# Kernel optimization log

Measured on AMD Instinct MI355X. Metric: run time of the kernel, lower is better.

## Reference

```python
import jax, jax.numpy as jnp
import numpy as np

B, S, D = 4, 2048, 1024
H, DK = 16, 64
NUM_BUCKETS = 32
MAX_DISTANCE = 128
EPS = 1e-6


def _relative_position_bucket(q_len, kv_len):
    # causal (bidirectional=False) T5 bucketization
    ctx = jnp.arange(q_len, dtype=jnp.int32)[:, None]
    mem = jnp.arange(kv_len, dtype=jnp.int32)[None, :]
    rp = mem - ctx                       # [q, kv]
    rp = -jnp.minimum(rp, 0)             # nonnegative distances to the past
    max_exact = NUM_BUCKETS // 2
    is_small = rp < max_exact
    rp_safe = jnp.maximum(rp, 1).astype(jnp.float32)
    large = max_exact + (
        jnp.log(rp_safe / max_exact) / np.log(MAX_DISTANCE / max_exact) * (NUM_BUCKETS - max_exact)
    ).astype(jnp.int32)
    large = jnp.minimum(large, NUM_BUCKETS - 1)
    return jnp.where(is_small, rp, large)  # [q, kv] int32 in [0, NUM_BUCKETS)


def setup_inputs() -> dict:
    key = jax.random.key(0)
    k1, k2, k3, k4 = jax.random.split(key, 4)
    hidden_states = jax.random.normal(k1, (B, S, D), dtype=jnp.float32)
    sequence_mask = jnp.ones((B, S), dtype=bool)
    rms_w = jnp.ones((D,), dtype=jnp.float32)
    W_qkv = jax.random.normal(k2, (D, 3 * H * DK), dtype=jnp.float32) * (D ** -0.5)
    W_o = jax.random.normal(k3, (H * DK, D), dtype=jnp.float32) * ((H * DK) ** -0.5)
    rel_bias = jax.random.normal(k4, (NUM_BUCKETS, H), dtype=jnp.float32)
    return {"hidden_states": hidden_states, "sequence_mask": sequence_mask,
            "rms_w": rms_w, "W_qkv": W_qkv, "W_o": W_o, "rel_bias": rel_bias}


def reference(hidden_states, sequence_mask, rms_w, W_qkv, W_o, rel_bias):
    # RMSNorm
    var = jnp.mean(hidden_states * hidden_states, axis=-1, keepdims=True)
    normed = hidden_states * jax.lax.rsqrt(var + EPS) * rms_w

    # QKV projection -> [B, S, 3, H, DK] -> [B, H, S, DK] each
    qkv = (normed @ W_qkv).reshape(B, S, 3, H, DK)
    q = jnp.transpose(qkv[:, :, 0], (0, 2, 1, 3))
    k = jnp.transpose(qkv[:, :, 1], (0, 2, 1, 3))
    v = jnp.transpose(qkv[:, :, 2], (0, 2, 1, 3))

    # relative position bias: gather [S,S,H] -> [1,H,S,S]
    bucket = _relative_position_bucket(S, S)
    pos_bias = jnp.transpose(rel_bias[bucket], (2, 0, 1))[None]

    # scores (note: T5 does NOT scale by 1/sqrt(dk))
    scores = jnp.einsum("bhqd,bhkd->bhqk", q, k) + pos_bias

    # causal mask combined with sequence mask (True = attend)
    causal = jnp.tril(jnp.ones((S, S), dtype=bool))
    mask = causal[None, None] & sequence_mask[:, None, None, :]
    scores = jnp.where(mask, scores, jnp.finfo(scores.dtype).min)

    attn = jax.nn.softmax(scores.astype(jnp.float32), axis=-1).astype(scores.dtype)
    # dropout p=0 / eval mode -> identity
    ctx = jnp.einsum("bhqk,bhkd->bhqd", attn, v)          # [B,H,S,DK]
    ctx = jnp.transpose(ctx, (0, 2, 1, 3)).reshape(B, S, H * DK)
    out = hidden_states + ctx @ W_o                        # residual
    return out
```

## Files before the change

kernel.cpp:

```cpp
#include <hip/hip_runtime.h>
#include <math.h>


typedef unsigned short ushort_t;
typedef __attribute__((ext_vector_type(8))) short bfrag;
typedef __attribute__((ext_vector_type(4))) float ffrag;

#define MFMA16(a, b, c) __builtin_amdgcn_mfma_f32_16x16x32_bf16((a), (b), (c), 0, 0, 0)

__device__ __forceinline__ void load_lds16(const ushort_t* g, ushort_t* l) {
  __builtin_amdgcn_global_load_lds(
      (const __attribute__((address_space(1))) unsigned int*)g,
      (__attribute__((address_space(3))) unsigned int*)l, 16, 0, 0);
}

__device__ __forceinline__ ushort_t f2bf(float f) {
  union { float f; unsigned u; } x; x.f = f;
  unsigned r = x.u + 0x7FFFu + ((x.u >> 16) & 1u);
  return (ushort_t)(r >> 16);
}
__device__ __forceinline__ float bf2f(ushort_t u) {
  union { unsigned u; float f; } x; x.u = ((unsigned)u) << 16; return x.f;
}
__device__ __forceinline__ unsigned pk2bf(float lo, float hi) {
  union { float f; unsigned u; } a, b; a.f = lo; b.f = hi;
  unsigned ra = a.u + 0x7FFFu + ((a.u >> 16) & 1u);
  unsigned rb = b.u + 0x7FFFu + ((b.u >> 16) & 1u);
  return (ra >> 16) | (rb & 0xFFFF0000u);
}

__global__ __launch_bounds__(256) void norm_cvt_kernel(
    const float* __restrict__ hidden, const float* __restrict__ rms_w,
    ushort_t* __restrict__ normed) {
  const int w = threadIdx.x >> 6, lane = threadIdx.x & 63;
  const int row = blockIdx.x * 4 + w;
  const float* p = hidden + (size_t)row * 1024;
  float4 v[4];
  float s = 0.f;
#pragma unroll
  for (int i = 0; i < 4; ++i) {
    v[i] = *(const float4*)(p + (lane + i * 64) * 4);
    s += v[i].x * v[i].x + v[i].y * v[i].y + v[i].z * v[i].z + v[i].w * v[i].w;
  }
#pragma unroll
  for (int off = 1; off < 64; off <<= 1) s += __shfl_xor(s, off, 64);
  const float scale = rsqrtf(s * (1.0f / 1024.0f) + 1e-6f);
#pragma unroll
  for (int i = 0; i < 4; ++i) {
    const int c0 = (lane + i * 64) * 4;
    float4 wv = *(const float4*)(rms_w + c0);
    ushort4 u;
    u.x = f2bf(v[i].x * scale * wv.x);
    u.y = f2bf(v[i].y * scale * wv.y);
    u.z = f2bf(v[i].z * scale * wv.z);
    u.w = f2bf(v[i].w * scale * wv.w);
    *(ushort4*)(normed + (size_t)row * 1024 + c0) = u;
  }
}

__global__ __launch_bounds__(256) void transpose_cvt_kernel(
    const float* __restrict__ in, ushort_t* __restrict__ out, int R, int C) {
  __shared__ float tile[32][33];
  const int r0 = blockIdx.y * 32, c0 = blockIdx.x * 32;
  const int tr = threadIdx.x >> 5, tc = threadIdx.x & 31;
#pragma unroll
  for (int i = 0; i < 32; i += 8)
    tile[tr + i][tc] = in[(size_t)(r0 + tr + i) * C + c0 + tc];
  __syncthreads();
#pragma unroll
  for (int i = 0; i < 32; i += 8)
    out[(size_t)(c0 + tr + i) * R + r0 + tc] = f2bf(tile[tc][tr + i]);
}

__global__ __launch_bounds__(256) void qkv_mfma_kernel(
    const ushort_t* __restrict__ A, const ushort_t* __restrict__ Bt,
    ushort_t* __restrict__ qbf, ushort_t* __restrict__ kbf,
    ushort_t* __restrict__ vtbf) {
  __shared__ ushort_t At[128 * 32];
  __shared__ ushort_t Bs[128 * 32];
  const int tid = threadIdx.x, w = tid >> 6, lane = tid & 63;
  const int quad = lane >> 4, ln = lane & 15;
  const int wr = w >> 1, wc = w & 1;
  const int m0 = blockIdx.y * 128, n0 = blockIdx.x * 128;
  const int srow = lane >> 2, scol = (lane & 3) * 8;

  ffrag acc[4][4];
#pragma unroll
  for (int i = 0; i < 4; ++i)
#pragma unroll
    for (int j = 0; j < 4; ++j) acc[i][j] = (ffrag)0.f;

  for (int kb = 0; kb < 1024; kb += 32) {
#pragma unroll
    for (int p = 0; p < 2; ++p) {
      load_lds16(A + (size_t)(m0 + (w * 2 + p) * 16 + srow) * 1024 + kb + scol,
                 At + (w * 2 + p) * 512);
      load_lds16(Bt + (size_t)(n0 + (w * 2 + p) * 16 + srow) * 1024 + kb + scol,
                 Bs + (w * 2 + p) * 512);
    }
    __syncthreads();
    bfrag a[4], b[4];
#pragma unroll
    for (int mi = 0; mi < 4; ++mi)
      a[mi] = *(const bfrag*)(At + (wr * 64 + mi * 16 + ln) * 32 + quad * 8);
#pragma unroll
    for (int ni = 0; ni < 4; ++ni)
      b[ni] = *(const bfrag*)(Bs + (wc * 64 + ni * 16 + ln) * 32 + quad * 8);
#pragma unroll
    for (int mi = 0; mi < 4; ++mi)
#pragma unroll
      for (int ni = 0; ni < 4; ++ni)
        acc[mi][ni] = MFMA16(a[mi], b[ni], acc[mi][ni]);
    __syncthreads();
  }

  const int b_idx = m0 >> 11;
  const int cbase = n0 + wc * 64 + ln;
#pragma unroll
  for (int mi = 0; mi < 4; ++mi) {
    const int sbase = (m0 & 2047) + wr * 64 + mi * 16 + quad * 4;
#pragma unroll
    for (int ni = 0; ni < 4; ++ni) {
      const int c = cbase + ni * 16;
      const int three = c >> 10, rem = c & 1023;
      const int h = rem >> 6, dk = rem & 63;
      if (three == 2) {
        ushort4 u;
        u.x = f2bf(acc[mi][ni][0]); u.y = f2bf(acc[mi][ni][1]);
        u.z = f2bf(acc[mi][ni][2]); u.w = f2bf(acc[mi][ni][3]);
        *(ushort4*)(vtbf + ((size_t)(b_idx * 16 + h) * 64 + dk) * 2048 + sbase) = u;
      } else {
        ushort_t* dst = (three == 0 ? qbf : kbf) +
                        ((size_t)(b_idx * 16 + h) * 2048 + sbase) * 64 + dk;
        dst[0]   = f2bf(acc[mi][ni][0]);
        dst[64]  = f2bf(acc[mi][ni][1]);
        dst[128] = f2bf(acc[mi][ni][2]);
        dst[192] = f2bf(acc[mi][ni][3]);
      }
    }
  }
}

__global__ __launch_bounds__(256) void attn_mfma_kernel(
    const ushort_t* __restrict__ qbf, const ushort_t* __restrict__ kbf,
    const ushort_t* __restrict__ vtbf, const float* __restrict__ rel_bias,
    ushort_t* __restrict__ ctx) {
  __shared__ ushort_t Kt[2][64][32];
  __shared__ ushort_t Vt[2][64][32];
  __shared__ ushort_t Pt[128][72];
  __shared__ ushort_t bias_t[2048];

  const int tid = threadIdx.x, w = tid >> 6, lane = tid & 63;
  const int quad = lane >> 4, ln = lane & 15;
  const int id = blockIdx.x;
  const int bh = id & 63;
  const int g = id >> 6;
  const int qb = (g < 4) ? (15 - 2 * g)
               : (g < 8) ? (2 * g - 8)
               : (g < 12) ? (30 - 2 * g)
                          : (2 * g - 23);
  const int h = bh & 15;

  for (int dist = tid; dist < 2048; dist += 256) {
    int bucket;
    if (dist < 16) bucket = dist;
    else {
      bucket = 16 + (int)(logf((float)dist * (1.0f / 16.0f)) * (16.0f / logf(8.0f)));
      if (bucket > 31) bucket = 31;
    }
    bias_t[dist] = f2bf(rel_bias[bucket * 16 + h]);
  }
  const float c31 = bf2f(f2bf(rel_bias[31 * 16 + h]));

  const int q0w = qb * 128 + w * 32;
  const size_t qrow = (size_t)bh * 2048 + q0w + ln;
  bfrag aq[2][2];
#pragma unroll
  for (int ni = 0; ni < 2; ++ni)
#pragma unroll
    for (int kf = 0; kf < 2; ++kf)
      aq[ni][kf] = *(const bfrag*)(qbf + (qrow + ni * 16) * 64 + kf * 32 + quad * 8);

  ffrag o[2][4];
  float m_run[2] = {-3.0e38f, -3.0e38f}, l_run[2] = {0.f, 0.f};
#pragma unroll
  for (int mo = 0; mo < 2; ++mo)
#pragma unroll
    for (int nd = 0; nd < 4; ++nd) o[mo][nd] = (ffrag)0.f;

  const int sidx = lane >> 2, scol8 = (lane & 3) * 8;
  const size_t khead = (size_t)bh * 2048 * 64;
  const int jmax = qb * 2 + 1;

  for (int j = 0; j <= jmax; ++j) {
    const int key0 = j * 64;
#pragma unroll
    for (int p = 0; p < 2; ++p) {
      const int idx = p * 4 + w, panel = idx >> 2, rb = idx & 3;
      load_lds16(kbf + khead + (size_t)(key0 + rb * 16 + sidx) * 64 + panel * 32 + scol8,
                 &Kt[0][0][0] + idx * 512);
      load_lds16(vtbf + khead + (size_t)(rb * 16 + sidx) * 2048 + key0 + panel * 32 + scol8,
                 &Vt[0][0][0] + idx * 512);
    }
    __syncthreads();

    if (key0 <= q0w + 31) {
      ffrag s[4][2];
#pragma unroll
      for (int mi = 0; mi < 4; ++mi)
#pragma unroll
        for (int ni = 0; ni < 2; ++ni) s[mi][ni] = (ffrag)0.f;
#pragma unroll
      for (int kf = 0; kf < 2; ++kf)
#pragma unroll
        for (int mi = 0; mi < 4; ++mi) {
          bfrag ak = *(const bfrag*)&Kt[kf][mi * 16 + ln][quad * 8];
          s[mi][0] = MFMA16(ak, aq[0][kf], s[mi][0]);
          s[mi][1] = MFMA16(ak, aq[1][kf], s[mi][1]);
        }

      float alpha[2];
      const bool fast = (key0 + 176 <= q0w);
      if (fast) {
#pragma unroll
        for (int ni = 0; ni < 2; ++ni) {
          float mx = s[0][ni][0];
#pragma unroll
          for (int mi = 0; mi < 4; ++mi)
#pragma unroll
            for (int r = 0; r < 4; ++r) mx = fmaxf(mx, s[mi][ni][r]);
          mx = fmaxf(mx, __shfl_xor(mx, 16, 64));
          mx = fmaxf(mx, __shfl_xor(mx, 32, 64));
          const float mnew = fmaxf(m_run[ni], mx + c31);
          alpha[ni] = __expf(m_run[ni] - mnew);
          const float sh = mnew - c31;
          float ps = 0.f;
#pragma unroll
          for (int mi = 0; mi < 4; ++mi)
#pragma unroll
            for (int r = 0; r < 4; ++r) {
              const float pv = __expf(s[mi][ni][r] - sh);
              s[mi][ni][r] = pv;
              ps += pv;
            }
          ps += __shfl_xor(ps, 16, 64);
          ps += __shfl_xor(ps, 32, 64);
          l_run[ni] = l_run[ni] * alpha[ni] + ps;
          m_run[ni] = mnew;
        }
      } else {
#pragma unroll
        for (int ni = 0; ni < 2; ++ni) {
          const int q = q0w + ni * 16 + ln;
          float mx = -3.0e38f;
#pragma unroll
          for (int mi = 0; mi < 4; ++mi) {
            const int keyb = key0 + mi * 16 + quad * 4;
#pragma unroll
            for (int r = 0; r < 4; ++r) {
              const int dist = q - (keyb + r);
              const float val =
                  (dist < 0) ? -3.0e38f : (s[mi][ni][r] + bf2f(bias_t[dist]));
              s[mi][ni][r] = val;
              mx = fmaxf(mx, val);
            }
          }
          mx = fmaxf(mx, __shfl_xor(mx, 16, 64));
          mx = fmaxf(mx, __shfl_xor(mx, 32, 64));
          const float mnew = fmaxf(m_run[ni], mx);
          alpha[ni] = __expf(m_run[ni] - mnew);
          float ps = 0.f;
#pragma unroll
          for (int mi = 0; mi < 4; ++mi)
#pragma unroll
            for (int r = 0; r < 4; ++r) {
              const float pv = __expf(s[mi][ni][r] - mnew);
              s[mi][ni][r] = pv;
              ps += pv;
            }
          ps += __shfl_xor(ps, 16, 64);
          ps += __shfl_xor(ps, 32, 64);
          l_run[ni] = l_run[ni] * alpha[ni] + ps;
          m_run[ni] = mnew;
        }
      }

#pragma unroll
      for (int ni = 0; ni < 2; ++ni) {
        ushort_t* prow = &Pt[w * 32 + ni * 16 + ln][0];
#pragma unroll
        for (int mi = 0; mi < 4; ++mi) {
          uint2 pk;
          pk.x = pk2bf(s[mi][ni][0], s[mi][ni][1]);
          pk.y = pk2bf(s[mi][ni][2], s[mi][ni][3]);
          *(uint2*)(prow + mi * 16 + quad * 4) = pk;
        }
      }

#pragma unroll
      for (int mo = 0; mo < 2; ++mo) {
#pragma unroll
        for (int r = 0; r < 4; ++r) {
          const float af = __shfl(alpha[mo], quad * 4 + r, 64);
#pragma unroll
          for (int nd = 0; nd < 4; ++nd) o[mo][nd][r] *= af;
        }
      }

#pragma unroll
      for (int kf = 0; kf < 2; ++kf) {
        bfrag ap0 = *(const bfrag*)&Pt[w * 32 + ln][kf * 32 + quad * 8];
        bfrag ap1 = *(const bfrag*)&Pt[w * 32 + 16 + ln][kf * 32 + quad * 8];
#pragma unroll
        for (int nd = 0; nd < 4; ++nd) {
          bfrag bv = *(const bfrag*)&Vt[kf][nd * 16 + ln][quad * 8];
          o[0][nd] = MFMA16(ap0, bv, o[0][nd]);
          o[1][nd] = MFMA16(ap1, bv, o[1][nd]);
        }
      }
    }
    __syncthreads();
  }

#pragma unroll
  for (int mo = 0; mo < 2; ++mo) {
    ffrag inv;
#pragma unroll
    for (int r = 0; r < 4; ++r)
      inv[r] = 1.0f / __shfl(l_run[mo], quad * 4 + r, 64);
    const int s0 = q0w + mo * 16 + quad * 4;
#pragma unroll
    for (int nd = 0; nd < 4; ++nd)
#pragma unroll
      for (int r = 0; r < 4; ++r)
        ctx[((size_t)(bh >> 4) * 2048 + s0 + r) * 1024 + h * 64 + nd * 16 + ln] =
            f2bf(o[mo][nd][r] * inv[r]);
  }
}

__global__ __launch_bounds__(256) void out_mfma_kernel(
    const ushort_t* __restrict__ A, const ushort_t* __restrict__ Bt,
    const float* __restrict__ hidden, float* __restrict__ out) {
  __shared__ ushort_t At[128 * 32];
  __shared__ ushort_t Bs[128 * 32];
  const int tid = threadIdx.x, w = tid >> 6, lane = tid & 63;
  const int quad = lane >> 4, ln = lane & 15;
  const int wr = w >> 1, wc = w & 1;
  const int m0 = blockIdx.y * 128, n0 = blockIdx.x * 128;
  const int srow = lane >> 2, scol = (lane & 3) * 8;

  ffrag acc[4][4];
#pragma unroll
  for (int i = 0; i < 4; ++i)
#pragma unroll
    for (int j = 0; j < 4; ++j) acc[i][j] = (ffrag)0.f;

  for (int kb = 0; kb < 1024; kb += 32) {
#pragma unroll
    for (int p = 0; p < 2; ++p) {
      load_lds16(A + (size_t)(m0 + (w * 2 + p) * 16 + srow) * 1024 + kb + scol,
                 At + (w * 2 + p) * 512);
      load_lds16(Bt + (size_t)(n0 + (w * 2 + p) * 16 + srow) * 1024 + kb + scol,
                 Bs + (w * 2 + p) * 512);
    }
    __syncthreads();
    bfrag a[4], b[4];
#pragma unroll
    for (int mi = 0; mi < 4; ++mi)
      a[mi] = *(const bfrag*)(At + (wr * 64 + mi * 16 + ln) * 32 + quad * 8);
#pragma unroll
    for (int ni = 0; ni < 4; ++ni)
      b[ni] = *(const bfrag*)(Bs + (wc * 64 + ni * 16 + ln) * 32 + quad * 8);
#pragma unroll
    for (int mi = 0; mi < 4; ++mi)
#pragma unroll
      for (int ni = 0; ni < 4; ++ni)
        acc[mi][ni] = MFMA16(a[mi], b[ni], acc[mi][ni]);
    __syncthreads();
  }
#pragma unroll
  for (int mi = 0; mi < 4; ++mi) {
    const int m = m0 + wr * 64 + mi * 16 + quad * 4;
#pragma unroll
    for (int ni = 0; ni < 4; ++ni) {
      const int c = n0 + wc * 64 + ni * 16 + ln;
#pragma unroll
      for (int r = 0; r < 4; ++r) {
        const size_t off = (size_t)(m + r) * 1024 + c;
        out[off] = acc[mi][ni][r] + hidden[off];
      }
    }
  }
}

extern "C" void kernel_launch(void* const* d_in, const int* in_sizes, int n_in,
                              void* d_out, int out_size, void* d_ws, size_t ws_size,
                              hipStream_t stream) {
  const size_t NORMED = (size_t)8192 * 1024;
  const size_t WQKVT  = (size_t)3072 * 1024;
  const size_t WOT    = (size_t)1024 * 1024;
  const size_t QKVE   = (size_t)64 * 2048 * 64;
  const size_t need = (NORMED + WQKVT + WOT + 3 * QKVE + NORMED) * 2;
  if (ws_size < need) return;

  const float* hidden   = (const float*)d_in[0];
  const float* rms_w    = (const float*)d_in[2];
  const float* Wqkv     = (const float*)d_in[3];
  const float* Wo       = (const float*)d_in[4];
  const float* rel_bias = (const float*)d_in[5];
  float* out = (float*)d_out;

  ushort_t* normed = (ushort_t*)d_ws;
  ushort_t* wqkvt  = normed + NORMED;
  ushort_t* wot    = wqkvt + WQKVT;
  ushort_t* qbf    = wot + WOT;
  ushort_t* kbf    = qbf + QKVE;
  ushort_t* vtbf   = kbf + QKVE;
  ushort_t* ctx    = vtbf + QKVE;

  norm_cvt_kernel<<<2048, 256, 0, stream>>>(hidden, rms_w, normed);
  transpose_cvt_kernel<<<dim3(96, 32), 256, 0, stream>>>(Wqkv, wqkvt, 1024, 3072);
  transpose_cvt_kernel<<<dim3(32, 32), 256, 0, stream>>>(Wo, wot, 1024, 1024);
  qkv_mfma_kernel<<<dim3(24, 64), 256, 0, stream>>>(normed, wqkvt, qbf, kbf, vtbf);
  attn_mfma_kernel<<<1024, 256, 0, stream>>>(qbf, kbf, vtbf, rel_bias, ctx);
  out_mfma_kernel<<<dim3(8, 64), 256, 0, stream>>>(ctx, wot, hidden, out);
}
```

Before: 308.0 us.

## Split long causal attention rows into KV chunks with a separate merge kernel

Query blocks 8-15 now have their key range split into two KV chunks, each handled by its own workgroup through a constant work-item table. The chunks write fp32 partial O, m and l, and a new merge kernel combines them into ctx. This evens out causal load imbalance and the tail. It also swaps the LDS bias table for register-resident bias values read through ds_bpermute, and XOR-swizzles the P tile in LDS to reduce bank conflicts. In exchange it adds an extra kernel launch, fp32 partial traffic and more per-element bias lookup instructions.

```diff
diff --git a/kernel.cpp b/kernel.cpp
--- a/kernel.cpp
+++ b/kernel.cpp
@@ -18,9 +18,6 @@
   union { float f; unsigned u; } x; x.f = f;
   unsigned r = x.u + 0x7FFFu + ((x.u >> 16) & 1u);
   return (ushort_t)(r >> 16);
-}
-__device__ __forceinline__ float bf2f(ushort_t u) {
-  union { unsigned u; float f; } x; x.u = ((unsigned)u) << 16; return x.f;
 }
 __device__ __forceinline__ unsigned pk2bf(float lo, float hi) {
   union { float f; unsigned u; } a, b; a.f = lo; b.f = hi;
@@ -141,36 +138,50 @@
   }
 }
 
-__global__ __launch_bounds__(256) void attn_mfma_kernel(
+__constant__ signed char IT[24][4] = {
+  {15, 0,16,14},{15,16,16,15},{ 7, 0,16,-1},
+  {14, 0,15,12},{14,15,15,13},
+  {13, 0,14,10},{13,14,14,11},{ 6, 0,14,-1},
+  {12, 0,13, 8},{12,13,13, 9},
+  {11, 0,12, 6},{11,12,12, 7},{ 5, 0,12,-1},
+  {10, 0,11, 4},{10,11,11, 5},
+  { 9, 0,10, 2},{ 9,10,10, 3},{ 4, 0,10,-1},
+  { 8, 0, 9, 0},{ 8, 9, 9, 1},
+  { 3, 0, 8,-1},{ 2, 0, 6,-1},{ 1, 0, 4,-1},{ 0, 0, 2,-1},
+};
+
+__global__ __launch_bounds__(256, 5) void attn_mfma_kernel(
     const ushort_t* __restrict__ qbf, const ushort_t* __restrict__ kbf,
     const ushort_t* __restrict__ vtbf, const float* __restrict__ rel_bias,
-    ushort_t* __restrict__ ctx) {
+    ushort_t* __restrict__ ctx, float* __restrict__ Opart,
+    float* __restrict__ mpart, float* __restrict__ lpart) {
   __shared__ ushort_t Kt[2][64][32];
   __shared__ ushort_t Vt[2][64][32];
-  __shared__ ushort_t Pt[128][72];
-  __shared__ ushort_t bias_t[2048];
+  __shared__ ushort_t Pt[128 * 64];
 
   const int tid = threadIdx.x, w = tid >> 6, lane = tid & 63;
   const int quad = lane >> 4, ln = lane & 15;
-  const int id = blockIdx.x;
-  const int bh = id & 63;
-  const int g = id >> 6;
-  const int qb = (g < 4) ? (15 - 2 * g)
-               : (g < 8) ? (2 * g - 8)
-               : (g < 12) ? (30 - 2 * g)
-                          : (2 * g - 23);
+  const int item = blockIdx.x >> 6, bh = blockIdx.x & 63;
+  const int qb = IT[item][0], k0 = IT[item][1], kn = IT[item][2];
+  const int slot = IT[item][3];
   const int h = bh & 15;
 
-  for (int dist = tid; dist < 2048; dist += 256) {
-    int bucket;
-    if (dist < 16) bucket = dist;
-    else {
-      bucket = 16 + (int)(logf((float)dist * (1.0f / 16.0f)) * (16.0f / logf(8.0f)));
-      if (bucket > 31) bucket = 31;
-    }
-    bias_t[dist] = f2bf(rel_bias[bucket * 16 + h]);
-  }
-  const float c31 = bf2f(f2bf(rel_bias[31 * 16 + h]));
+  float bias_v0, bias_v1;
+  {
+#pragma unroll
+    for (int half = 0; half < 2; ++half) {
+      const int d = half * 64 + lane;
+      int bucket;
+      if (d < 16) bucket = d;
+      else {
+        bucket = 16 + (int)(logf((float)d * (1.0f / 16.0f)) * (16.0f / logf(8.0f)));
+        if (bucket > 31) bucket = 31;
+      }
+      const float bv = rel_bias[bucket * 16 + h];
+      if (half == 0) bias_v0 = bv; else bias_v1 = bv;
+    }
+  }
+  const float c31 = __shfl(bias_v1, 49, 64);
 
   const int q0w = qb * 128 + w * 32;
   const size_t qrow = (size_t)bh * 2048 + q0w + ln;
@@ -190,9 +201,9 @@
 
   const int sidx = lane >> 2, scol8 = (lane & 3) * 8;
   const size_t khead = (size_t)bh * 2048 * 64;
-  const int jmax = qb * 2 + 1;
-
-  for (int j = 0; j <= jmax; ++j) {
+  const int swz = ln & 7;
+
+  for (int j = k0; j < k0 + kn; ++j) {
     const int key0 = j * 64;
 #pragma unroll
     for (int p = 0; p < 2; ++p) {
@@ -259,8 +270,11 @@
 #pragma unroll
             for (int r = 0; r < 4; ++r) {
               const int dist = q - (keyb + r);
-              const float val =
-                  (dist < 0) ? -3.0e38f : (s[mi][ni][r] + bf2f(bias_t[dist]));
+              const int d2 = (dist < 127) ? dist : 127;
+              const int b0 = __builtin_amdgcn_ds_bpermute(d2 << 2, __float_as_int(bias_v0));
+              const int b1 = __builtin_amdgcn_ds_bpermute((d2 - 64) << 2, __float_as_int(bias_v1));
+              const float bias = __int_as_float(d2 < 64 ? b0 : b1);
+              const float val = (dist < 0) ? -3.0e38f : (s[mi][ni][r] + bias);
               s[mi][ni][r] = val;
               mx = fmaxf(mx, val);
             }
@@ -287,13 +301,14 @@
 
 #pragma unroll
       for (int ni = 0; ni < 2; ++ni) {
-        ushort_t* prow = &Pt[w * 32 + ni * 16 + ln][0];
+        ushort_t* prow = &Pt[(w * 32 + ni * 16 + ln) * 64];
 #pragma unroll
         for (int mi = 0; mi < 4; ++mi) {
           uint2 pk;
           pk.x = pk2bf(s[mi][ni][0], s[mi][ni][1]);
           pk.y = pk2bf(s[mi][ni][2], s[mi][ni][3]);
-          *(uint2*)(prow + mi * 16 + quad * 4) = pk;
+          const int u = 2 * mi + (quad >> 1);
+          *(uint2*)(prow + ((u ^ swz) * 8 + (quad & 1) * 4)) = pk;
         }
       }
 
@@ -309,8 +324,9 @@
 
 #pragma unroll
       for (int kf = 0; kf < 2; ++kf) {
-        bfrag ap0 = *(const bfrag*)&Pt[w * 32 + ln][kf * 32 + quad * 8];
-        bfrag ap1 = *(const bfrag*)&Pt[w * 32 + 16 + ln][kf * 32 + quad * 8];
+        const int ur = (kf * 4 + quad);
+        bfrag ap0 = *(const bfrag*)&Pt[(w * 32 + ln) * 64 + (ur ^ swz) * 8];
+        bfrag ap1 = *(const bfrag*)&Pt[(w * 32 + 16 + ln) * 64 + (ur ^ swz) * 8];
 #pragma unroll
         for (int nd = 0; nd < 4; ++nd) {
           bfrag bv = *(const bfrag*)&Vt[kf][nd * 16 + ln][quad * 8];
@@ -322,19 +338,69 @@
     __syncthreads();
   }
 
-#pragma unroll
-  for (int mo = 0; mo < 2; ++mo) {
-    ffrag inv;
-#pragma unroll
-    for (int r = 0; r < 4; ++r)
-      inv[r] = 1.0f / __shfl(l_run[mo], quad * 4 + r, 64);
-    const int s0 = q0w + mo * 16 + quad * 4;
-#pragma unroll
-    for (int nd = 0; nd < 4; ++nd)
+  if (slot >= 0) {
+    if (quad == 0) {
+#pragma unroll
+      for (int ni = 0; ni < 2; ++ni) {
+        const int row = w * 32 + ni * 16 + ln;
+        mpart[((size_t)bh * 16 + slot) * 128 + row] = m_run[ni];
+        lpart[((size_t)bh * 16 + slot) * 128 + row] = l_run[ni];
+      }
+    }
+#pragma unroll
+    for (int mo = 0; mo < 2; ++mo)
+#pragma unroll
+      for (int nd = 0; nd < 4; ++nd)
+#pragma unroll
+        for (int r = 0; r < 4; ++r)
+          Opart[(((size_t)bh * 16 + slot) * 128 + w * 32 + mo * 16 + quad * 4 + r) * 64 +
+                nd * 16 + ln] = o[mo][nd][r];
+  } else {
+#pragma unroll
+    for (int mo = 0; mo < 2; ++mo) {
+      ffrag inv;
 #pragma unroll
       for (int r = 0; r < 4; ++r)
-        ctx[((size_t)(bh >> 4) * 2048 + s0 + r) * 1024 + h * 64 + nd * 16 + ln] =
-            f2bf(o[mo][nd][r] * inv[r]);
+        inv[r] = 1.0f / __shfl(l_run[mo], quad * 4 + r, 64);
+      const int s0 = q0w + mo * 16 + quad * 4;
+#pragma unroll
+      for (int nd = 0; nd < 4; ++nd)
+#pragma unroll
+        for (int r = 0; r < 4; ++r)
+          ctx[((size_t)(bh >> 4) * 2048 + s0 + r) * 1024 + h * 64 + nd * 16 + ln] =
+              f2bf(o[mo][nd][r] * inv[r]);
+    }
+  }
+}
+
+__global__ __launch_bounds__(256) void attn_merge_kernel(
+    const float* __restrict__ Opart, const float* __restrict__ mpart,
+    const float* __restrict__ lpart, ushort_t* __restrict__ ctx) {
+  const int bh = blockIdx.x & 63, qi = blockIdx.x >> 6;
+  const int qb = 8 + qi, sA = qi * 2, sB = sA + 1;
+  const int t = threadIdx.x;
+  const int r = t >> 1, c0 = (t & 1) * 32;
+  const size_t baseA = ((size_t)bh * 16 + sA) * 128 + r;
+  const size_t baseB = ((size_t)bh * 16 + sB) * 128 + r;
+  const float mA = mpart[baseA], mB = mpart[baseB];
+  const float lA = lpart[baseA], lB = lpart[baseB];
+  const float m = fmaxf(mA, mB);
+  const float aA = __expf(mA - m), aB = __expf(mB - m);
+  const float inv = 1.0f / (aA * lA + aB * lB);
+  const float* OA = Opart + baseA * 64 + c0;
+  const float* OB = Opart + baseB * 64 + c0;
+  ushort_t* dst = ctx + ((size_t)(bh >> 4) * 2048 + qb * 128 + r) * 1024 +
+                  (bh & 15) * 64 + c0;
+#pragma unroll
+  for (int i = 0; i < 8; ++i) {
+    float4 oa = *(const float4*)(OA + i * 4);
+    float4 ob = *(const float4*)(OB + i * 4);
+    ushort4 u;
+    u.x = f2bf((aA * oa.x + aB * ob.x) * inv);
+    u.y = f2bf((aA * oa.y + aB * ob.y) * inv);
+    u.z = f2bf((aA * oa.z + aB * ob.z) * inv);
+    u.w = f2bf((aA * oa.w + aB * ob.w) * inv);
+    *(ushort4*)(dst + i * 4) = u;
   }
 }
 
@@ -400,7 +466,10 @@
   const size_t WQKVT  = (size_t)3072 * 1024;
   const size_t WOT    = (size_t)1024 * 1024;
   const size_t QKVE   = (size_t)64 * 2048 * 64;
-  const size_t need = (NORMED + WQKVT + WOT + 3 * QKVE + NORMED) * 2;
+  const size_t USH    = NORMED + WQKVT + WOT + 3 * QKVE + NORMED;
+  const size_t OPARTE = (size_t)64 * 16 * 128 * 64;
+  const size_t MLE    = (size_t)64 * 16 * 128;
+  const size_t need = USH * 2 + (OPARTE + 2 * MLE) * 4;
   if (ws_size < need) return;
 
   const float* hidden   = (const float*)d_in[0];
@@ -417,11 +486,16 @@
   ushort_t* kbf    = qbf + QKVE;
   ushort_t* vtbf   = kbf + QKVE;
   ushort_t* ctx    = vtbf + QKVE;
+  float* Opart = (float*)(ctx + NORMED);
+  float* mpart = Opart + OPARTE;
+  float* lpart = mpart + MLE;
 
   norm_cvt_kernel<<<2048, 256, 0, stream>>>(hidden, rms_w, normed);
   transpose_cvt_kernel<<<dim3(96, 32), 256, 0, stream>>>(Wqkv, wqkvt, 1024, 3072);
   transpose_cvt_kernel<<<dim3(32, 32), 256, 0, stream>>>(Wo, wot, 1024, 1024);
   qkv_mfma_kernel<<<dim3(24, 64), 256, 0, stream>>>(normed, wqkvt, qbf, kbf, vtbf);
-  attn_mfma_kernel<<<1024, 256, 0, stream>>>(qbf, kbf, vtbf, rel_bias, ctx);
+  attn_mfma_kernel<<<1536, 256, 0, stream>>>(qbf, kbf, vtbf, rel_bias, ctx,
+                                             Opart, mpart, lpart);
+  attn_merge_kernel<<<512, 256, 0, stream>>>(Opart, mpart, lpart, ctx);
   out_mfma_kernel<<<dim3(8, 64), 256, 0, stream>>>(ctx, wot, hidden, out);
 }
```

Measured after the change: 503.9 us. 63.6% more time.
